# Kernel tuning notes

Measured on AMD Instinct MI355X. Metric: run time of the kernel, lower is better.

The kernel has to match this reference:

```python
import jax, jax.numpy as jnp
import numpy as np

B, L, DIM = 16, 131072, 9  # batch, audio samples, 1 fundamental + 8 harmonics
SR = 22050.0
SINE_AMP = 0.1
NOISE_STD = 0.003


def setup_inputs() -> dict:
    key = jax.random.key(0)
    k1, k2, k3, k4 = jax.random.split(key, 4)
    u = jax.random.uniform(k1, (B, L, 1), dtype=jnp.float32)
    voiced = jax.random.uniform(k2, (B, L, 1), dtype=jnp.float32) > 0.3
    f0 = jnp.where(voiced, 100.0 + 300.0 * u, 0.0)  # Hz, 0 where unvoiced
    rand_ini = jax.random.uniform(k3, (B, DIM), dtype=jnp.float32)
    rand_ini = rand_ini.at[:, 0].set(0.0)  # first harmonic gets no random phase
    noise_z = jax.random.normal(k4, (B, L, DIM), dtype=jnp.float32)
    return {"f0": f0, "rand_ini": rand_ini, "noise_z": noise_z}


def reference(f0, rand_ini, noise_z):
    dim = noise_z.shape[-1]
    two_pi = 2.0 * jnp.pi
    # harmonic multiples of f0: (B, L, dim)
    k = jnp.arange(1, dim + 1, dtype=f0.dtype)
    fn = f0 * k
    # normalized per-step phase increment in [0, 1)
    rad = jnp.mod(fn / SR, 1.0)
    rad = rad.at[:, 0, :].add(rand_ini)  # random initial phase per harmonic
    # wrap-around detection: cumulative phase mod 1 decreases at a wrap
    tmp_over_one = jnp.mod(jnp.cumsum(rad, axis=1), 1.0)
    wrap = (tmp_over_one[:, 1:, :] - tmp_over_one[:, :-1, :]) < 0.0
    cumsum_shift = jnp.concatenate(
        [jnp.zeros_like(rad[:, :1, :]), jnp.where(wrap, -1.0, 0.0).astype(rad.dtype)],
        axis=1,
    )
    sines = jnp.sin(jnp.cumsum(rad + cumsum_shift, axis=1) * two_pi)
    sine_waves = sines * SINE_AMP
    # voiced/unvoiced mask from fundamental f0
    uv = (f0 > 0.0).astype(f0.dtype)  # (B, L, 1)
    noise_amp = uv * NOISE_STD + (1.0 - uv) * (SINE_AMP / 3.0)
    noise = noise_amp * noise_z
    sine_waves = sine_waves * uv + noise
    return sine_waves, uv, noise
```

## Files before the change

### kernel.cpp

```cpp
#include <hip/hip_runtime.h>
#include <math.h>


#define Bq 16
#define Lq 131072
#define DIMq 9
#define CHUNK 2048
#define NCHUNK (Lq / CHUNK)
#define NT 256
#define PT 8
#define Q4 (CHUNK * DIMq / 4 / NT)

__global__ void __launch_bounds__(NT) k_partials(const float* __restrict__ f0,
                                                 double* __restrict__ part) {
  int b = blockIdx.x >> 6, tid = threadIdx.x, lane = tid & 63, wave = tid >> 6;
  const float* p = f0 + (size_t)b * Lq + (size_t)(blockIdx.x & 63) * CHUNK + tid * PT;
  float4 x = *(const float4*)p;
  float4 y = *(const float4*)(p + 4);
  double s = ((double)x.x + (double)x.y) + ((double)x.z + (double)x.w) +
             ((double)y.x + (double)y.y) + ((double)y.z + (double)y.w);
#pragma unroll
  for (int d = 32; d > 0; d >>= 1) s += __shfl_xor(s, d, 64);
  __shared__ double ws[NT / 64];
  if (lane == 0) ws[wave] = s;
  __syncthreads();
  if (tid == 0) part[blockIdx.x] = ws[0] + ws[1] + ws[2] + ws[3];
}

__global__ void __launch_bounds__(NT) k_main(
    const float* __restrict__ f0, const float* __restrict__ rini,
    const float* __restrict__ nz, const double* __restrict__ part,
    float* __restrict__ out0, float* __restrict__ out1,
    float* __restrict__ out2) {
  int bc = blockIdx.x;
  int b = bc >> 6, c = bc & 63;
  int tid = threadIdx.x, lane = tid & 63, wave = tid >> 6;
  size_t t0g = (size_t)b * Lq + (size_t)c * CHUNK;

  __shared__ float p1s[CHUNK + CHUNK / 8];
  __shared__ float nmps[CHUNK + CHUNK / 8];
  __shared__ float inis[DIMq];
  __shared__ double wsum[NT / 64];

  const float* fp = f0 + t0g + tid * PT;
  float4 fa = *(const float4*)fp;
  float4 fb = *(const float4*)(fp + 4);
  float fv[PT] = {fa.x, fa.y, fa.z, fa.w, fb.x, fb.y, fb.z, fb.w};
  double run = 0.0, inc[PT];
#pragma unroll
  for (int j = 0; j < PT; ++j) { run += (double)fv[j]; inc[j] = run; }
  double tot = run;
#pragma unroll
  for (int d = 1; d < 64; d <<= 1) {
    double o = __shfl_up(tot, d, 64);
    if (lane >= d) tot += o;
  }
  if (lane == 63) wsum[wave] = tot;
  if (tid < DIMq) inis[tid] = rini[b * DIMq + tid];
  __syncthreads();
  double pv = (lane < c) ? part[(b << 6) + lane] : 0.0;
#pragma unroll
  for (int d = 32; d > 0; d >>= 1) pv += __shfl_xor(pv, d, 64);
  double wpre = 0.0;
  for (int w = 0; w < wave; ++w) wpre += wsum[w];
  double base = pv + wpre + (tot - run);
  const double invsr = 1.0 / 22050.0;
  const float nampU = (float)(0.1 / 3.0);
  float uvv[PT];
#pragma unroll
  for (int j = 0; j < PT; ++j) {
    double ph = (base + inc[j]) * invsr;
    ph -= floor(ph);
    int t = tid * PT + j;
    p1s[t + (t >> 3)] = (float)ph;
    bool v = fv[j] > 0.0f;
    nmps[t + (t >> 3)] = v ? 0.003f : -nampU;
    uvv[j] = v ? 1.0f : 0.0f;
  }
  *(float4*)(out1 + t0g + tid * PT) = make_float4(uvv[0], uvv[1], uvv[2], uvv[3]);
  *(float4*)(out1 + t0g + tid * PT + 4) = make_float4(uvv[4], uvv[5], uvv[6], uvv[7]);
  __syncthreads();

  const float4* nzc = (const float4*)(nz + t0g * DIMq);
  float4* o0c = (float4*)(out0 + t0g * DIMq);
  float4* o2c = (float4*)(out2 + t0g * DIMq);

  auto gen = [&](int t, int d, float nzv, float& r0, float& r2) {
    int ti = t + (t >> 3);
    float p1 = p1s[ti], nm = nmps[ti];
    float ph = (float)(d + 1) * p1 + inis[d];
    ph -= floorf(ph);
    float s = __builtin_amdgcn_sinf(ph) * 0.1f;
    float noise = fabsf(nm) * nzv;
    r2 = noise;
    r0 = (nm > 0.0f) ? s + noise : noise;
  };

#pragma unroll 6
  for (int w = 0; w < Q4; ++w) {
    int q = w * NT + tid;
    int e = q * 4;
    int t = (int)(((unsigned)e * 7282u) >> 16);
    int d = e - t * 9;
    float4 nzv = nzc[q];
    float4 r0, r2;
    gen(t, d, nzv.x, r0.x, r2.x); if (++d == 9) { d = 0; ++t; }
    gen(t, d, nzv.y, r0.y, r2.y); if (++d == 9) { d = 0; ++t; }
    gen(t, d, nzv.z, r0.z, r2.z); if (++d == 9) { d = 0; ++t; }
    gen(t, d, nzv.w, r0.w, r2.w);
    o0c[q] = r0;
    o2c[q] = r2;
  }
}

extern "C" void kernel_launch(void* const* d_in, const int* in_sizes, int n_in,
                              void* d_out, int out_size, void* d_ws, size_t ws_size,
                              hipStream_t stream) {
  const float* f0 = (const float*)d_in[0];
  const float* rini = (const float*)d_in[1];
  const float* nz = (const float*)d_in[2];
  float* out = (float*)d_out;
  float* out0 = out;
  float* out1 = out + (size_t)Bq * Lq * DIMq;
  float* out2 = out1 + (size_t)Bq * Lq;
  double* part = (double*)d_ws;

  k_partials<<<Bq * NCHUNK, NT, 0, stream>>>(f0, part);
  k_main<<<Bq * NCHUNK, NT, 0, stream>>>(f0, rini, nz, part, out0, out1, out2);
}
```

Before: 47.97 us.

## Fuse partial-sum and main kernels via decoupled block aggregate flags

```diff
diff --git a/kernel.cpp b/kernel.cpp
--- a/kernel.cpp
+++ b/kernel.cpp
@@ -7,31 +7,18 @@
 #define DIMq 9
 #define CHUNK 2048
 #define NCHUNK (Lq / CHUNK)
+#define NBLK (Bq * NCHUNK)
 #define NT 256
 #define PT 8
 #define Q4 (CHUNK * DIMq / 4 / NT)
 
-__global__ void __launch_bounds__(NT) k_partials(const float* __restrict__ f0,
-                                                 double* __restrict__ part) {
-  int b = blockIdx.x >> 6, tid = threadIdx.x, lane = tid & 63, wave = tid >> 6;
-  const float* p = f0 + (size_t)b * Lq + (size_t)(blockIdx.x & 63) * CHUNK + tid * PT;
-  float4 x = *(const float4*)p;
-  float4 y = *(const float4*)(p + 4);
-  double s = ((double)x.x + (double)x.y) + ((double)x.z + (double)x.w) +
-             ((double)y.x + (double)y.y) + ((double)y.z + (double)y.w);
-#pragma unroll
-  for (int d = 32; d > 0; d >>= 1) s += __shfl_xor(s, d, 64);
-  __shared__ double ws[NT / 64];
-  if (lane == 0) ws[wave] = s;
-  __syncthreads();
-  if (tid == 0) part[blockIdx.x] = ws[0] + ws[1] + ws[2] + ws[3];
-}
+typedef float f32x4 __attribute__((ext_vector_type(4)));
 
-__global__ void __launch_bounds__(NT) k_main(
+__global__ void __launch_bounds__(NT, 4) k_fused(
     const float* __restrict__ f0, const float* __restrict__ rini,
-    const float* __restrict__ nz, const double* __restrict__ part,
-    float* __restrict__ out0, float* __restrict__ out1,
-    float* __restrict__ out2) {
+    const float* __restrict__ nz, double* __restrict__ agg,
+    unsigned* __restrict__ flags, float* __restrict__ out0,
+    float* __restrict__ out1, float* __restrict__ out2) {
   int bc = blockIdx.x;
   int b = bc >> 6, c = bc & 63;
   int tid = threadIdx.x, lane = tid & 63, wave = tid >> 6;
@@ -42,9 +29,9 @@
   __shared__ float inis[DIMq];
   __shared__ double wsum[NT / 64];
 
-  const float* fp = f0 + t0g + tid * PT;
-  float4 fa = *(const float4*)fp;
-  float4 fb = *(const float4*)(fp + 4);
+  const f32x4* fp = (const f32x4*)(f0 + t0g + tid * PT);
+  f32x4 fa = fp[0];
+  f32x4 fb = fp[1];
   float fv[PT] = {fa.x, fa.y, fa.z, fa.w, fb.x, fb.y, fb.z, fb.w};
   double run = 0.0, inc[PT];
 #pragma unroll
@@ -58,12 +45,27 @@
   if (lane == 63) wsum[wave] = tot;
   if (tid < DIMq) inis[tid] = rini[b * DIMq + tid];
   __syncthreads();
-  double pv = (lane < c) ? part[(b << 6) + lane] : 0.0;
+
+  if (tid == 0) {
+    double a = (wsum[0] + wsum[1]) + (wsum[2] + wsum[3]);
+    agg[bc] = a;
+    __hip_atomic_store(&flags[bc], 1u, __ATOMIC_RELEASE, __HIP_MEMORY_SCOPE_AGENT);
+  }
+
+  double pv = 0.0;
+  if (lane < c) {
+    const unsigned* fl = flags + (b << 6) + lane;
+    while (__hip_atomic_load(fl, __ATOMIC_ACQUIRE, __HIP_MEMORY_SCOPE_AGENT) != 1u)
+      __builtin_amdgcn_s_sleep(1);
+    pv = __hip_atomic_load(&agg[(b << 6) + lane], __ATOMIC_RELAXED,
+                           __HIP_MEMORY_SCOPE_AGENT);
+  }
 #pragma unroll
   for (int d = 32; d > 0; d >>= 1) pv += __shfl_xor(pv, d, 64);
   double wpre = 0.0;
   for (int w = 0; w < wave; ++w) wpre += wsum[w];
   double base = pv + wpre + (tot - run);
+
   const double invsr = 1.0 / 22050.0;
   const float nampU = (float)(0.1 / 3.0);
   float uvv[PT];
@@ -77,23 +79,28 @@
     nmps[t + (t >> 3)] = v ? 0.003f : -nampU;
     uvv[j] = v ? 1.0f : 0.0f;
   }
-  *(float4*)(out1 + t0g + tid * PT) = make_float4(uvv[0], uvv[1], uvv[2], uvv[3]);
-  *(float4*)(out1 + t0g + tid * PT + 4) = make_float4(uvv[4], uvv[5], uvv[6], uvv[7]);
+  f32x4 u0 = {uvv[0], uvv[1], uvv[2], uvv[3]};
+  f32x4 u1 = {uvv[4], uvv[5], uvv[6], uvv[7]};
+  __builtin_nontemporal_store(u0, (f32x4*)(out1 + t0g + tid * PT));
+  __builtin_nontemporal_store(u1, (f32x4*)(out1 + t0g + tid * PT + 4));
   __syncthreads();
 
-  const float4* nzc = (const float4*)(nz + t0g * DIMq);
-  float4* o0c = (float4*)(out0 + t0g * DIMq);
-  float4* o2c = (float4*)(out2 + t0g * DIMq);
+  const f32x4* nzc = (const f32x4*)(nz + t0g * DIMq);
+  f32x4* o0c = (f32x4*)(out0 + t0g * DIMq);
+  f32x4* o2c = (f32x4*)(out2 + t0g * DIMq);
 
-  auto gen = [&](int t, int d, float nzv, float& r0, float& r2) {
+  struct R { float r0, r2; };
+  auto gen = [&](int t, int d, float nzv) -> R {
     int ti = t + (t >> 3);
     float p1 = p1s[ti], nm = nmps[ti];
     float ph = (float)(d + 1) * p1 + inis[d];
     ph -= floorf(ph);
     float s = __builtin_amdgcn_sinf(ph) * 0.1f;
     float noise = fabsf(nm) * nzv;
-    r2 = noise;
-    r0 = (nm > 0.0f) ? s + noise : noise;
+    R r;
+    r.r2 = noise;
+    r.r0 = (nm > 0.0f) ? s + noise : noise;
+    return r;
   };
 
 #pragma unroll 6
@@ -102,14 +109,15 @@
     int e = q * 4;
     int t = (int)(((unsigned)e * 7282u) >> 16);
     int d = e - t * 9;
-    float4 nzv = nzc[q];
-    float4 r0, r2;
-    gen(t, d, nzv.x, r0.x, r2.x); if (++d == 9) { d = 0; ++t; }
-    gen(t, d, nzv.y, r0.y, r2.y); if (++d == 9) { d = 0; ++t; }
-    gen(t, d, nzv.z, r0.z, r2.z); if (++d == 9) { d = 0; ++t; }
-    gen(t, d, nzv.w, r0.w, r2.w);
-    o0c[q] = r0;
-    o2c[q] = r2;
+    f32x4 nzv = __builtin_nontemporal_load(&nzc[q]);
+    R a = gen(t, d, nzv.x); if (++d == 9) { d = 0; ++t; }
+    R bb = gen(t, d, nzv.y); if (++d == 9) { d = 0; ++t; }
+    R cc = gen(t, d, nzv.z); if (++d == 9) { d = 0; ++t; }
+    R dd = gen(t, d, nzv.w);
+    f32x4 r0 = {a.r0, bb.r0, cc.r0, dd.r0};
+    f32x4 r2 = {a.r2, bb.r2, cc.r2, dd.r2};
+    __builtin_nontemporal_store(r0, &o0c[q]);
+    __builtin_nontemporal_store(r2, &o2c[q]);
   }
 }
 
@@ -123,8 +131,9 @@
   float* out0 = out;
   float* out1 = out + (size_t)Bq * Lq * DIMq;
   float* out2 = out1 + (size_t)Bq * Lq;
-  double* part = (double*)d_ws;
+  double* agg = (double*)d_ws;
+  unsigned* flags = (unsigned*)((char*)d_ws + NBLK * sizeof(double));
 
-  k_partials<<<Bq * NCHUNK, NT, 0, stream>>>(f0, part);
-  k_main<<<Bq * NCHUNK, NT, 0, stream>>>(f0, rini, nz, part, out0, out1, out2);
+  (void)hipMemsetAsync(flags, 0, NBLK * sizeof(unsigned), stream);
+  k_fused<<<NBLK, NT, 0, stream>>>(f0, rini, nz, agg, flags, out0, out1, out2);
 }
```

New measurement: 150.9 us. 215% more time.
